# Optimization experiments

Hardware: AMD Instinct MI355X
Metric: run time of the kernel (lower is better)

The kernel has to match this reference:

```python
import jax, jax.numpy as jnp
import numpy as np

N, E, CIN, CHID, DIM, KS = 6000, 192000, 32, 64, 3, 5
K = KS ** DIM          # 125 total spline kernel weights
S = 2 ** DIM           # 8 nonzero linear B-spline basis products per edge


def spline_conv(x, edge_index, pseudo, W, root, bias):
    """SplineConv, degree-1 open B-spline, mean aggregation, root weight + bias.
    x: [N, Cin], edge_index: [2, E], pseudo: [E, DIM] in [0,1],
    W: [K, Cin, Cout], root: [Cin, Cout], bias: [Cout].
    """
    src, dst = edge_index[0], edge_index[1]
    cin = x.shape[1]
    # open spline: KS-1 intervals over [0,1]
    u = pseudo * (KS - 1)                               # [E, DIM]
    i0 = jnp.clip(jnp.floor(u), 0, KS - 2).astype(jnp.int32)
    frac = u - i0                                       # [E, DIM]
    bits = (jnp.arange(S)[:, None] >> jnp.arange(DIM)[None, :]) & 1   # [S, DIM]
    strides = KS ** jnp.arange(DIM - 1, -1, -1)         # row-major flattening
    idx = jnp.sum((i0[:, None, :] + bits[None, :, :]) * strides, axis=-1)  # [E, S]
    basis = jnp.prod(jnp.where(bits[None, :, :] == 1,
                               frac[:, None, :], 1.0 - frac[:, None, :]), axis=-1)  # [E, S]
    x_j = x[src]                                        # gather: [E, Cin]
    vals = (basis[..., None] * x_j[:, None, :]).reshape(E * S, cin)
    keys = (dst[:, None] * K + idx).reshape(E * S)
    # bucket basis-weighted source features per (dst node, kernel index)
    T = jax.ops.segment_sum(vals, keys, num_segments=N * K).reshape(N, K, cin)
    out = jnp.einsum('nki,kio->no', T, W)               # [N, Cout]
    deg = jax.ops.segment_sum(jnp.ones((E,), jnp.float32), dst, num_segments=N)
    out = out / jnp.maximum(deg, 1.0)[:, None]          # mean aggregation
    return out + x @ root + bias


def _conv_params(key, cin):
    k1, k2 = jax.random.split(key)
    w_scale = 1.0 / np.sqrt(cin * S)
    W = jax.random.normal(k1, (K, cin, CHID), jnp.float32) * w_scale
    root = jax.random.normal(k2, (cin, CHID), jnp.float32) * (1.0 / np.sqrt(cin))
    b = jnp.zeros((CHID,), jnp.float32)
    return W, root, b


def setup_inputs() -> dict:
    key = jax.random.key(0)
    ks = jax.random.split(key, 10)
    inp = {
        'x': jax.random.normal(ks[0], (N, CIN), jnp.float32),
        'hidden': jax.random.normal(ks[1], (N, CHID), jnp.float32),
        'edge_index': jax.random.randint(ks[2], (2, E), 0, N, dtype=jnp.int32),
        'edge_attr': jax.random.uniform(ks[3], (E, DIM), jnp.float32),
    }
    for i, (name, cin) in enumerate([('xr', CIN), ('hr', CHID), ('xz', CIN),
                                     ('hz', CHID), ('xn', CIN), ('hn', CHID)]):
        W, root, b = _conv_params(ks[4 + i], cin)
        inp[f'W_{name}'] = W
        inp[f'root_{name}'] = root
        inp[f'b_{name}'] = b
    return inp


def reference(x, hidden, edge_index, edge_attr,
              W_xr, root_xr, b_xr, W_hr, root_hr, b_hr,
              W_xz, root_xz, b_xz, W_hz, root_hz, b_hz,
              W_xn, root_xn, b_xn, W_hn, root_hn, b_hn):
    hr_out = spline_conv(hidden, edge_index, edge_attr, W_hr, root_hr, b_hr)
    r = jax.nn.sigmoid(spline_conv(x, edge_index, edge_attr, W_xr, root_xr, b_xr) + hr_out)
    z = jax.nn.sigmoid(spline_conv(x, edge_index, edge_attr, W_xz, root_xz, b_xz)
                       + spline_conv(hidden, edge_index, edge_attr, W_hz, root_hz, b_hz))
    # NOTE: the original torch forward reuses self.hr (not self.hn) here; replicated faithfully.
    n = jnp.tanh(spline_conv(x, edge_index, edge_attr, W_xn, root_xn, b_xn) + r * hr_out)
    h_new = (1.0 - z) * n + z * hidden
    return h_new
```

## Files before the change

kernel.cpp:

```cpp
#include <hip/hip_runtime.h>
#include <math.h>

#define NN_   6000
#define EE_   192000
#define CIN_  32
#define CHID_ 64
#define KK_   125
#define EB_   32
#define CH1_  4
#define CH2_  8
#define CPB_  16
#define MTILE_ 192

static __device__ __forceinline__ unsigned short f2bf(float f) {
    unsigned int u = __builtin_bit_cast(unsigned int, f);
    u += 0x7fff + ((u >> 16) & 1);
    return (unsigned short)(u >> 16);
}
static __device__ __forceinline__ float bf2f(unsigned short h) {
    unsigned int u = ((unsigned int)h) << 16;
    return __builtin_bit_cast(float, u);
}

template<int N> static __device__ __forceinline__ void vwait() {
    asm volatile("s_waitcnt vmcnt(%0)" :: "n"(N) : "memory");
    __builtin_amdgcn_sched_barrier(0);
}

#define PK1_ (192 * KK_ * CIN_)
#define PK2_ (128 * KK_ * CHID_)
#define CB_  ((EE_ + 255) / 256)
__global__ __launch_bounds__(256) void count_pack_kernel(
    const int* __restrict__ ei, int* __restrict__ deg,
    const float* __restrict__ W_xr, const float* __restrict__ W_xz,
    const float* __restrict__ W_xn, const float* __restrict__ W_hr,
    const float* __restrict__ W_hz,
    unsigned short* __restrict__ B1t, unsigned short* __restrict__ B2t)
{
    const int b = blockIdx.x;
    if (b < CB_) {
        int e = b * 256 + threadIdx.x;
        if (e < EE_) atomicAdd(&deg[ei[EE_ + e]], 1);
        return;
    }
    int gid = (b - CB_) * 256 + threadIdx.x;
    if (gid < PK1_) {
        int n  = gid / (KK_ * CIN_);
        int kk = gid % (KK_ * CIN_);
        int conv = n >> 6, o = n & 63;
        const float* W = (conv == 0) ? W_xr : ((conv == 1) ? W_xz : W_xn);
        B1t[gid] = f2bf(W[(size_t)kk * 64 + o]);
    } else if (gid < PK1_ + PK2_) {
        int g2 = gid - PK1_;
        int n  = g2 / (KK_ * CHID_);
        int kk = g2 % (KK_ * CHID_);
        int conv = n >> 6, o = n & 63;
        const float* W = (conv == 0) ? W_hr : W_hz;
        B2t[g2] = f2bf(W[(size_t)kk * 64 + o]);
    }
}

__global__ __launch_bounds__(1024) void scan_kernel(
    const int* __restrict__ deg, int* __restrict__ offs, int* __restrict__ cursor)
{
    __shared__ int part[1024];
    const int tid = threadIdx.x;
    const int CH = (NN_ + 1023) / 1024;
    const int base = tid * CH;
    int loc[CH];
    int s = 0;
#pragma unroll
    for (int i = 0; i < CH; ++i) {
        int v = (base + i < NN_) ? deg[base + i] : 0;
        loc[i] = s; s += v;
    }
    part[tid] = s;
    __syncthreads();
    for (int off = 1; off < 1024; off <<= 1) {
        int v = (tid >= off) ? part[tid - off] : 0;
        __syncthreads();
        part[tid] += v;
        __syncthreads();
    }
    const int pre = (tid > 0) ? part[tid - 1] : 0;
#pragma unroll
    for (int i = 0; i < CH; ++i) {
        if (base + i < NN_) {
            offs[base + i]   = pre + loc[i];
            cursor[base + i] = pre + loc[i];
        }
    }
    if (tid == 1023) offs[NN_] = part[1023];
}

__global__ __launch_bounds__(256) void prep_kernel(
    const int* __restrict__ ei, const float* __restrict__ attr,
    int* __restrict__ cursor, float4* __restrict__ meta_s, int* __restrict__ src_s)
{
    int e = blockIdx.x * 256 + threadIdx.x;
    if (e >= EE_) return;
    const int dst = ei[EE_ + e];
    const int p   = atomicAdd(&cursor[dst], 1);
    float f[3]; int i0[3];
#pragma unroll
    for (int d = 0; d < 3; ++d) {
        float u  = attr[e * 3 + d] * 4.0f;
        float fl = floorf(u);
        fl = fminf(fmaxf(fl, 0.0f), 3.0f);
        i0[d] = (int)fl;
        f[d]  = u - fl;
    }
    meta_s[p] = make_float4(f[0], f[1], f[2],
        __int_as_float(i0[0] * 25 + i0[1] * 5 + i0[2]));
    src_s[p] = ei[e];
}

template<int C>
__global__ __launch_bounds__(256) void build_T_kernel(
    const float4* __restrict__ meta_s, const int* __restrict__ src_s,
    const float* __restrict__ feat, const int* __restrict__ offs,
    unsigned short* __restrict__ Tb)
{
    constexpr int MP  = 40;
    constexpr int CT  = C / 16;
    constexpr int CPT = C / 8;
    using bf16x8 = __attribute__((ext_vector_type(8))) short;
    using f32x4  = __attribute__((ext_vector_type(4))) float;

    __shared__ __align__(16) unsigned short Mt [128 * MP];
    __shared__ __align__(16) unsigned short fbT[C   * MP];
    __shared__ int s_src[EB_];

    const int tid  = threadIdx.x;
    const int wave = tid >> 6;
    const int lane = tid & 63;
    const int quad = lane >> 4;
    const int l16  = lane & 15;
    const int node = blockIdx.x;

    for (int i = tid; i < C * MP / 8; i += 256)
        ((uint4*)fbT)[i] = make_uint4(0u, 0u, 0u, 0u);

    const int j0 = offs[node], j1 = offs[node + 1];

    f32x4 acc[2][CT];
#pragma unroll
    for (int t = 0; t < 2; ++t)
#pragma unroll
        for (int ct = 0; ct < CT; ++ct) acc[t][ct] = (f32x4){0.f, 0.f, 0.f, 0.f};

    for (int jb = j0; jb < j1; jb += EB_) {
        const int m = min(EB_, j1 - jb);

        __syncthreads();
        for (int i = tid; i < 128 * MP / 8; i += 256)
            ((uint4*)Mt)[i] = make_uint4(0u, 0u, 0u, 0u);
        if (tid < m) s_src[tid] = src_s[jb + tid];
        __syncthreads();

        if (tid < m) {
            const float4 mt = meta_s[jb + tid];
            const int base = __float_as_int(mt.w);
            const float f0 = mt.x, f1 = mt.y, f2 = mt.z;
            const float g0 = 1.f - f0, g1 = 1.f - f1, g2 = 1.f - f2;
            const float bb[8] = {g0*g1*g2, f0*g1*g2, g0*f1*g2, f0*f1*g2,
                                 g0*g1*f2, f0*g1*f2, g0*f1*f2, f0*f1*f2};
            const int oc[8] = {0, 25, 5, 30, 1, 26, 6, 31};
#pragma unroll
            for (int s = 0; s < 8; ++s)
                Mt[(base + oc[s]) * MP + tid] = f2bf(bb[s]);
        }
        {
            const int e = tid >> 3, cg = (tid & 7) * CPT;
            if (e < m) {
                const float* fr = &feat[(size_t)s_src[e] * C + cg];
#pragma unroll
                for (int c4 = 0; c4 < CPT; c4 += 4) {
                    float4 v = *(const float4*)(fr + c4);
                    fbT[(cg + c4 + 0) * MP + e] = f2bf(v.x);
                    fbT[(cg + c4 + 1) * MP + e] = f2bf(v.y);
                    fbT[(cg + c4 + 2) * MP + e] = f2bf(v.z);
                    fbT[(cg + c4 + 3) * MP + e] = f2bf(v.w);
                }
            }
        }
        __syncthreads();

        bf16x8 a0 = *(const bf16x8*)&Mt[((wave * 2 + 0) * 16 + l16) * MP + quad * 8];
        bf16x8 a1 = *(const bf16x8*)&Mt[((wave * 2 + 1) * 16 + l16) * MP + quad * 8];
#pragma unroll
        for (int ct = 0; ct < CT; ++ct) {
            bf16x8 b = *(const bf16x8*)&fbT[(ct * 16 + l16) * MP + quad * 8];
            acc[0][ct] = __builtin_amdgcn_mfma_f32_16x16x32_bf16(a0, b, acc[0][ct], 0, 0, 0);
            acc[1][ct] = __builtin_amdgcn_mfma_f32_16x16x32_bf16(a1, b, acc[1][ct], 0, 0, 0);
        }
    }

    unsigned short* To = Tb + (size_t)node * (KK_ * C);
#pragma unroll
    for (int t = 0; t < 2; ++t) {
        const int rbase = (wave * 2 + t) * 16 + quad * 4;
#pragma unroll
        for (int ct = 0; ct < CT; ++ct) {
#pragma unroll
            for (int r = 0; r < 4; ++r) {
                const int R = rbase + r;
                if (R < KK_) To[R * C + ct * 16 + l16] = f2bf(acc[t][ct][r]);
            }
        }
    }
}

template<int NT, int NTF, int CPB, int LW>
static __device__ __forceinline__ void gemm_body(
    unsigned short* arena,
    const unsigned short* __restrict__ A, const unsigned short* __restrict__ Bt,
    const unsigned short* __restrict__ zp,
    unsigned short* __restrict__ P, int M, int Kd, int chunk, int zhalf)
{
    constexpr int COLS   = 64;
    constexpr int RF     = 3;
    constexpr int NFRAG  = NT / 16;
    constexpr int CSP    = NT + 8;
    constexpr int ASH    = MTILE_ * COLS;
    constexpr int SLOT   = ASH + 128 * COLS;
    constexpr int AUNITS = MTILE_ * COLS / 8;
    constexpr int BUNITS = NT * COLS / 8;

    using bf16x8 = __attribute__((ext_vector_type(8))) short;
    using f32x4  = __attribute__((ext_vector_type(4))) float;

    const int tid  = threadIdx.x;
    const int wave = tid >> 6;
    const int lane = tid & 63;
    const int quad = lane >> 4;
    const int l16  = lane & 15;
    const int m0   = blockIdx.x * MTILE_;
    const unsigned short* Bp = Bt + (size_t)zhalf * NT * Kd;
    const int kbase = chunk * CPB * COLS;
    const int ccmax = min(CPB, (Kd - kbase + COLS - 1) / COLS);

    f32x4 acc[RF][NFRAG];
#pragma unroll
    for (int t = 0; t < RF; ++t)
#pragma unroll
        for (int f = 0; f < NFRAG; ++f) acc[t][f] = (f32x4){0.f, 0.f, 0.f, 0.f};

    auto STAGE = [&](int cc, int slot) {
        unsigned short* Abuf = arena + slot * SLOT;
        unsigned short* Bbuf = Abuf + ASH;
        const int k0 = kbase + cc * COLS;
#pragma unroll
        for (int i = 0; i < AUNITS / 256; ++i) {
            const int u    = tid + i * 256;
            const int row  = u >> 3;
            const int gblk = (u & 7) ^ (row & 7);
            const int k    = k0 + gblk * 8;
            const unsigned short* g = (k + 8 <= Kd)
                ? A + (size_t)(m0 + row) * Kd + k
                : zp + (u & 3) * 8;
            __builtin_amdgcn_global_load_lds(
                (const __attribute__((address_space(1))) void*)g,
                (__attribute__((address_space(3))) void*)(Abuf + u * 8),
                16, 0, 0);
        }
#pragma unroll
        for (int i = 0; i < BUNITS / 256; ++i) {
            const int u    = tid + i * 256;
            const int row  = u >> 3;
            const int gblk = (u & 7) ^ (row & 7);
            const unsigned short* g = Bp + (size_t)row * Kd + k0 + gblk * 8;
            __builtin_amdgcn_global_load_lds(
                (const __attribute__((address_space(1))) void*)g,
                (__attribute__((address_space(3))) void*)(Bbuf + u * 8),
                16, 0, 0);
        }
    };

    STAGE(0, 0);
    STAGE(1, 1);

    for (int cc = 0; cc < ccmax; ++cc) {
        asm volatile("" ::: "memory");
        __builtin_amdgcn_s_barrier();
        if (cc + 2 < ccmax) STAGE(cc + 2, (cc + 2) % 3);
        const int ahead = min(2, ccmax - 1 - cc);
        if      (ahead == 2) vwait<2 * LW>();
        else if (ahead == 1) vwait<LW>();
        else                 vwait<0>();
        __builtin_amdgcn_s_barrier();
        asm volatile("" ::: "memory");

        const unsigned short* Ac = arena + (cc % 3) * SLOT;
        const unsigned short* Bc = Ac + ASH;
#pragma unroll
        for (int s = 0; s < 2; ++s) {
            bf16x8 av[RF];
#pragma unroll
            for (int t = 0; t < RF; ++t) {
                const int row = (wave * RF + t) * 16 + l16;
                av[t] = *(const bf16x8*)
                    &Ac[row * COLS + (((s * 4 + quad) ^ (l16 & 7)) * 8)];
            }
#pragma unroll
            for (int f = 0; f < NFRAG; ++f) {
                bf16x8 bv = *(const bf16x8*)
                    &Bc[(f * 16 + l16) * COLS + (((s * 4 + quad) ^ (l16 & 7)) * 8)];
#pragma unroll
                for (int t = 0; t < RF; ++t)
                    acc[t][f] = __builtin_amdgcn_mfma_f32_16x16x32_bf16(
                        av[t], bv, acc[t][f], 0, 0, 0);
            }
        }
    }

    unsigned short* Cs = arena;
    unsigned short* Pc = P + ((size_t)chunk * M + m0) * NTF + zhalf * NT;
#pragma unroll
    for (int p = 0; p < 3; ++p) {
        __syncthreads();
#pragma unroll
        for (int t = 0; t < RF; ++t) {
            const int fr = wave * RF + t;
            if ((fr >> 2) == p) {
                const int rb = (fr & 3) * 16 + quad * 4;
#pragma unroll
                for (int f = 0; f < NFRAG; ++f) {
                    const int col = f * 16 + l16;
#pragma unroll
                    for (int r = 0; r < 4; ++r)
                        Cs[(rb + r) * CSP + col] = f2bf(acc[t][f][r]);
                }
            }
        }
        __syncthreads();
        constexpr int UNITS = 64 * NT / 8;
        for (int u = tid; u < UNITS; u += 256) {
            const int row = (u * 8) / NT, col = (u * 8) % NT;
            if (m0 + p * 64 + row < M)
                *(uint4*)&Pc[(size_t)(p * 64 + row) * NTF + col] =
                    *(const uint4*)&Cs[row * CSP + col];
        }
    }
}

__global__ __launch_bounds__(256) void gemm_all_kernel(
    const unsigned short* __restrict__ Tx, const unsigned short* __restrict__ B1t,
    unsigned short* __restrict__ P1,
    const unsigned short* __restrict__ Th, const unsigned short* __restrict__ B2t,
    unsigned short* __restrict__ P2, const unsigned short* __restrict__ zp)
{
    __shared__ __align__(16) unsigned short arena[3 * 20480];
    const int y = blockIdx.y;
    if (y < CH2_) {
        gemm_body<128, 128, CPB_, 10>(arena, Th, B2t, zp, P2, NN_, KK_ * CHID_, y, 0);
    } else {
        const int g = y - CH2_;
        gemm_body<96, 192, CPB_, 9>(arena, Tx, B1t, zp, P1, NN_, KK_ * CIN_, g >> 1, g & 1);
    }
}

__global__ __launch_bounds__(256) void epilogue_kernel(
    const unsigned short* __restrict__ P1, const unsigned short* __restrict__ P2,
    const int* __restrict__ offs,
    const float* __restrict__ x, const float* __restrict__ hidden,
    const float* __restrict__ root_xr, const float* __restrict__ root_hr,
    const float* __restrict__ root_xz, const float* __restrict__ root_hz,
    const float* __restrict__ root_xn,
    const float* __restrict__ b_xr, const float* __restrict__ b_hr,
    const float* __restrict__ b_xz, const float* __restrict__ b_hz,
    const float* __restrict__ b_xn,
    float* __restrict__ out)
{
    __shared__ float xsh[4][32];
    __shared__ float hsh[4][64];
    const int w = threadIdx.x >> 6;
    const int o = threadIdx.x & 63;
    const int m = blockIdx.x * 4 + w;
    if (m >= NN_) return;

    if (o < 32) xsh[w][o] = x[(size_t)m * 32 + o];
    const float hval = hidden[(size_t)m * 64 + o];
    hsh[w][o] = hval;

    float axr = 0.f, axz = 0.f, axn = 0.f;
#pragma unroll
    for (int c = 0; c < CH1_; ++c) {
        const unsigned short* p = P1 + ((size_t)c * NN_ + m) * 192;
        axr += bf2f(p[o]); axz += bf2f(p[64 + o]); axn += bf2f(p[128 + o]);
    }
    float ahr = 0.f, ahz = 0.f;
#pragma unroll
    for (int c = 0; c < CH2_; ++c) {
        const unsigned short* p = P2 + ((size_t)c * NN_ + m) * 128;
        ahr += bf2f(p[o]); ahz += bf2f(p[64 + o]);
    }

    const int   dg   = offs[m + 1] - offs[m];
    const float dinv = 1.0f / fmaxf((float)dg, 1.0f);
    axr *= dinv; axz *= dinv; axn *= dinv; ahr *= dinv; ahz *= dinv;

    float sxr = 0.f, sxz = 0.f, sxn = 0.f;
#pragma unroll
    for (int c = 0; c < CIN_; ++c) {
        float xv = xsh[w][c];
        sxr += xv * root_xr[c * 64 + o];
        sxz += xv * root_xz[c * 64 + o];
        sxn += xv * root_xn[c * 64 + o];
    }
    float shr = 0.f, shz = 0.f;
#pragma unroll
    for (int c = 0; c < CHID_; ++c) {
        float hv = hsh[w][c];
        shr += hv * root_hr[c * 64 + o];
        shz += hv * root_hz[c * 64 + o];
    }

    const float conv_xr = axr + sxr + b_xr[o];
    const float conv_xz = axz + sxz + b_xz[o];
    const float conv_xn = axn + sxn + b_xn[o];
    const float hr_out  = ahr + shr + b_hr[o];
    const float conv_hz = ahz + shz + b_hz[o];

    const float rg = 1.0f / (1.0f + expf(-(conv_xr + hr_out)));
    const float zg = 1.0f / (1.0f + expf(-(conv_xz + conv_hz)));
    const float ng = tanhf(conv_xn + rg * hr_out);
    out[(size_t)m * 64 + o] = (1.0f - zg) * ng + zg * hval;
}

extern "C" void kernel_launch(void* const* d_in, const int* in_sizes, int n_in,
                              void* d_out, int out_size, void* d_ws, size_t ws_size,
                              hipStream_t stream)
{
    const float* x       = (const float*)d_in[0];
    const float* hidden  = (const float*)d_in[1];
    const int*   ei      = (const int*)  d_in[2];
    const float* attr    = (const float*)d_in[3];
    const float* W_xr    = (const float*)d_in[4];
    const float* root_xr = (const float*)d_in[5];
    const float* b_xr    = (const float*)d_in[6];
    const float* W_hr    = (const float*)d_in[7];
    const float* root_hr = (const float*)d_in[8];
    const float* b_hr    = (const float*)d_in[9];
    const float* W_xz    = (const float*)d_in[10];
    const float* root_xz = (const float*)d_in[11];
    const float* b_xz    = (const float*)d_in[12];
    const float* W_hz    = (const float*)d_in[13];
    const float* root_hz = (const float*)d_in[14];
    const float* b_hz    = (const float*)d_in[15];
    const float* W_xn    = (const float*)d_in[16];
    const float* root_xn = (const float*)d_in[17];
    const float* b_xn    = (const float*)d_in[18];
    float* out = (float*)d_out;

    char* w = (char*)d_ws;
    unsigned short* Tx  = (unsigned short*)w; w += (size_t)NN_ * KK_ * CIN_  * 2;
    unsigned short* Th  = (unsigned short*)w; w += (size_t)NN_ * KK_ * CHID_ * 2;
    unsigned short* B1t = (unsigned short*)w; w += (size_t)192 * KK_ * CIN_  * 2;
    unsigned short* B2t = (unsigned short*)w; w += (size_t)128 * KK_ * CHID_ * 2;
    unsigned short* P1  = (unsigned short*)w; w += (size_t)CH1_ * NN_ * 192 * 2;
    unsigned short* P2  = (unsigned short*)w; w += (size_t)CH2_ * NN_ * 128 * 2;
    float4* meta_s = (float4*)w; w += (size_t)EE_ * 16;
    int* src_s  = (int*)w;   w += (size_t)EE_ * 4;
    int* deg    = (int*)w;   w += (size_t)NN_ * 4;
    int* offs   = (int*)w;   w += (size_t)(NN_ + 4) * 4;
    int* cursor = (int*)w;   w += (size_t)NN_ * 4;
    unsigned short* zpad = (unsigned short*)w; w += 256;

    const int MT = (NN_ + MTILE_ - 1) / MTILE_;

    hipMemsetAsync(deg, 0, (size_t)NN_ * 4, stream);
    hipMemsetAsync(zpad, 0, 256, stream);

    const int PACKB = (PK1_ + PK2_ + 255) / 256;
    count_pack_kernel<<<CB_ + PACKB, 256, 0, stream>>>(
        ei, deg, W_xr, W_xz, W_xn, W_hr, W_hz, B1t, B2t);

    scan_kernel<<<1, 1024, 0, stream>>>(deg, offs, cursor);
    prep_kernel<<<(EE_ + 255) / 256, 256, 0, stream>>>(ei, attr, cursor, meta_s, src_s);

    build_T_kernel<CHID_><<<NN_, 256, 0, stream>>>(meta_s, src_s, hidden, offs, Th);
    build_T_kernel<CIN_><<<NN_, 256, 0, stream>>>(meta_s, src_s, x, offs, Tx);

    gemm_all_kernel<<<dim3(MT, CH2_ + 2 * CH1_), 256, 0, stream>>>(
        Tx, B1t, P1, Th, B2t, P2, zpad);

    epilogue_kernel<<<(NN_ + 3) / 4, 256, 0, stream>>>(
        P1, P2, offs, x, hidden,
        root_xr, root_hr, root_xz, root_hz, root_xn,
        b_xr, b_hr, b_xz, b_hz, b_xn, out);
}
```

Baseline: 245.2 us.

## Pad atomic counters, parallelize basis scatter, switch GEMM to double-buffered pipeline

Degree and cursor counters are spaced 16 ints apart so the atomics for neighbouring nodes stop contending on the same cache line. In build_T, basis weights are first staged in shared memory, and the 8 scatter writes per edge are spread over 8 threads instead of one loop per thread; one barrier is merged away. The GEMM moves from a 3-slot to a 2-slot LDS pipeline with one stage of prefetch, adds s_setprio around the MFMA section, and adds a trailing barrier. This cuts LDS use (possibly raising occupancy) but shortens the prefetch distance, and the padding adds a larger memset.

```diff
diff --git a/kernel.cpp b/kernel.cpp
--- a/kernel.cpp
+++ b/kernel.cpp
@@ -11,6 +11,7 @@
 #define CH2_  8
 #define CPB_  16
 #define MTILE_ 192
+#define DSTR_ 16
 
 static __device__ __forceinline__ unsigned short f2bf(float f) {
     unsigned int u = __builtin_bit_cast(unsigned int, f);
@@ -40,7 +41,7 @@
     const int b = blockIdx.x;
     if (b < CB_) {
         int e = b * 256 + threadIdx.x;
-        if (e < EE_) atomicAdd(&deg[ei[EE_ + e]], 1);
+        if (e < EE_) atomicAdd(&deg[ei[EE_ + e] * DSTR_], 1);
         return;
     }
     int gid = (b - CB_) * 256 + threadIdx.x;
@@ -71,7 +72,7 @@
     int s = 0;
 #pragma unroll
     for (int i = 0; i < CH; ++i) {
-        int v = (base + i < NN_) ? deg[base + i] : 0;
+        int v = (base + i < NN_) ? deg[(base + i) * DSTR_] : 0;
         loc[i] = s; s += v;
     }
     part[tid] = s;
@@ -86,8 +87,8 @@
 #pragma unroll
     for (int i = 0; i < CH; ++i) {
         if (base + i < NN_) {
-            offs[base + i]   = pre + loc[i];
-            cursor[base + i] = pre + loc[i];
+            offs[base + i]            = pre + loc[i];
+            cursor[(base + i) * DSTR_] = pre + loc[i];
         }
     }
     if (tid == 1023) offs[NN_] = part[1023];
@@ -100,7 +101,7 @@
     int e = blockIdx.x * 256 + threadIdx.x;
     if (e >= EE_) return;
     const int dst = ei[EE_ + e];
-    const int p   = atomicAdd(&cursor[dst], 1);
+    const int p   = atomicAdd(&cursor[dst * DSTR_], 1);
     float f[3]; int i0[3];
 #pragma unroll
     for (int d = 0; d < 3; ++d) {
@@ -129,7 +130,9 @@
 
     __shared__ __align__(16) unsigned short Mt [128 * MP];
     __shared__ __align__(16) unsigned short fbT[C   * MP];
-    __shared__ int s_src[EB_];
+    __shared__ int   s_src[EB_];
+    __shared__ int   s_cell[EB_];
+    __shared__ float s_basis[EB_ * 8];
 
     const int tid  = threadIdx.x;
     const int wave = tid >> 6;
@@ -155,20 +158,26 @@
         __syncthreads();
         for (int i = tid; i < 128 * MP / 8; i += 256)
             ((uint4*)Mt)[i] = make_uint4(0u, 0u, 0u, 0u);
-        if (tid < m) s_src[tid] = src_s[jb + tid];
-        __syncthreads();
-
         if (tid < m) {
             const float4 mt = meta_s[jb + tid];
-            const int base = __float_as_int(mt.w);
+            s_src[tid]  = src_s[jb + tid];
+            s_cell[tid] = __float_as_int(mt.w);
             const float f0 = mt.x, f1 = mt.y, f2 = mt.z;
             const float g0 = 1.f - f0, g1 = 1.f - f1, g2 = 1.f - f2;
-            const float bb[8] = {g0*g1*g2, f0*g1*g2, g0*f1*g2, f0*f1*g2,
-                                 g0*g1*f2, f0*g1*f2, g0*f1*f2, f0*f1*f2};
-            const int oc[8] = {0, 25, 5, 30, 1, 26, 6, 31};
-#pragma unroll
-            for (int s = 0; s < 8; ++s)
-                Mt[(base + oc[s]) * MP + tid] = f2bf(bb[s]);
+            float4 blo = make_float4(g0*g1*g2, f0*g1*g2, g0*f1*g2, f0*f1*g2);
+            float4 bhi = make_float4(g0*g1*f2, f0*g1*f2, g0*f1*f2, f0*f1*f2);
+            *(float4*)&s_basis[tid * 8]     = blo;
+            *(float4*)&s_basis[tid * 8 + 4] = bhi;
+        }
+        __syncthreads();
+
+        {
+            const int e = tid >> 3, s = tid & 7;
+            if (e < m) {
+                const int cell = s_cell[e] + 25 * (s & 1)
+                               + 5 * ((s >> 1) & 1) + ((s >> 2) & 1);
+                Mt[cell * MP + e] = f2bf(s_basis[e * 8 + s]);
+            }
         }
         {
             const int e = tid >> 3, cg = (tid & 7) * CPT;
@@ -278,21 +287,16 @@
     };
 
     STAGE(0, 0);
-    STAGE(1, 1);
 
     for (int cc = 0; cc < ccmax; ++cc) {
-        asm volatile("" ::: "memory");
-        __builtin_amdgcn_s_barrier();
-        if (cc + 2 < ccmax) STAGE(cc + 2, (cc + 2) % 3);
-        const int ahead = min(2, ccmax - 1 - cc);
-        if      (ahead == 2) vwait<2 * LW>();
-        else if (ahead == 1) vwait<LW>();
-        else                 vwait<0>();
+        if (cc + 1 < ccmax) { STAGE(cc + 1, (cc + 1) & 1); vwait<LW>(); }
+        else                { vwait<0>(); }
         __builtin_amdgcn_s_barrier();
         asm volatile("" ::: "memory");
 
-        const unsigned short* Ac = arena + (cc % 3) * SLOT;
+        const unsigned short* Ac = arena + (cc & 1) * SLOT;
         const unsigned short* Bc = Ac + ASH;
+        __builtin_amdgcn_s_setprio(1);
 #pragma unroll
         for (int s = 0; s < 2; ++s) {
             bf16x8 av[RF];
@@ -312,6 +316,10 @@
                         av[t], bv, acc[t][f], 0, 0, 0);
             }
         }
+        __builtin_amdgcn_s_setprio(0);
+        asm volatile("" ::: "memory");
+        __builtin_amdgcn_s_barrier();
+        asm volatile("" ::: "memory");
     }
 
     unsigned short* Cs = arena;
@@ -350,7 +358,7 @@
     const unsigned short* __restrict__ Th, const unsigned short* __restrict__ B2t,
     unsigned short* __restrict__ P2, const unsigned short* __restrict__ zp)
 {
-    __shared__ __align__(16) unsigned short arena[3 * 20480];
+    __shared__ __align__(16) unsigned short arena[2 * 20480];
     const int y = blockIdx.y;
     if (y < CH2_) {
         gemm_body<128, 128, CPB_, 10>(arena, Th, B2t, zp, P2, NN_, KK_ * CHID_, y, 0);
@@ -462,14 +470,14 @@
     unsigned short* P2  = (unsigned short*)w; w += (size_t)CH2_ * NN_ * 128 * 2;
     float4* meta_s = (float4*)w; w += (size_t)EE_ * 16;
     int* src_s  = (int*)w;   w += (size_t)EE_ * 4;
-    int* deg    = (int*)w;   w += (size_t)NN_ * 4;
+    int* deg    = (int*)w;   w += (size_t)NN_ * DSTR_ * 4;
     int* offs   = (int*)w;   w += (size_t)(NN_ + 4) * 4;
-    int* cursor = (int*)w;   w += (size_t)NN_ * 4;
+    int* cursor = (int*)w;   w += (size_t)NN_ * DSTR_ * 4;
     unsigned short* zpad = (unsigned short*)w; w += 256;
 
     const int MT = (NN_ + MTILE_ - 1) / MTILE_;
 
-    hipMemsetAsync(deg, 0, (size_t)NN_ * 4, stream);
+    hipMemsetAsync(deg, 0, (size_t)NN_ * DSTR_ * 4, stream);
     hipMemsetAsync(zpad, 0, 256, stream);
 
     const int PACKB = (PK1_ + PK2_ + 255) / 256;
```

Result: no change. 250.1 us (+2.0%).

## Shrink GEMM M-tile to 128 with double buffering and tile-transpose weight packing

Applied to the files above, without the earlier changes.

The GEMM M-tile drops from 192 to 128 rows (RF 3 to 2) and the LDS pipeline goes from three stages to two, so the arena shrinks and occupancy or block count can rise. MFMA sections are wrapped in s_setprio, and an extra barrier now ends each k-iteration. Separately, weight packing now transposes 64-row tiles through shared memory with coalesced float4 reads and uint4 writes, replacing the strided per-element gather. The trade-off is less prefetch depth and more barriers in exchange for more parallel blocks.

```diff
diff --git a/kernel.cpp b/kernel.cpp
--- a/kernel.cpp
+++ b/kernel.cpp
@@ -10,7 +10,7 @@
 #define CH1_  4
 #define CH2_  8
 #define CPB_  16
-#define MTILE_ 192
+#define MTILE_ 128
 
 static __device__ __forceinline__ unsigned short f2bf(float f) {
     unsigned int u = __builtin_bit_cast(unsigned int, f);
@@ -27,8 +27,11 @@
     __builtin_amdgcn_sched_barrier(0);
 }
 
-#define PK1_ (192 * KK_ * CIN_)
-#define PK2_ (128 * KK_ * CHID_)
+#define RX_  (KK_ * CIN_)
+#define RH_  (KK_ * CHID_)
+#define NB1_ ((RX_ + 63) / 64)
+#define NB2_ (RH_ / 64)
+#define PACKB_ (3 * NB1_ + 2 * NB2_)
 #define CB_  ((EE_ + 255) / 256)
 __global__ __launch_bounds__(256) void count_pack_kernel(
     const int* __restrict__ ei, int* __restrict__ deg,
@@ -37,26 +40,49 @@
     const float* __restrict__ W_hz,
     unsigned short* __restrict__ B1t, unsigned short* __restrict__ B2t)
 {
+    __shared__ float ts[64][65];
     const int b = blockIdx.x;
+    const int tid = threadIdx.x;
     if (b < CB_) {
-        int e = b * 256 + threadIdx.x;
+        int e = b * 256 + tid;
         if (e < EE_) atomicAdd(&deg[ei[EE_ + e]], 1);
         return;
     }
-    int gid = (b - CB_) * 256 + threadIdx.x;
-    if (gid < PK1_) {
-        int n  = gid / (KK_ * CIN_);
-        int kk = gid % (KK_ * CIN_);
-        int conv = n >> 6, o = n & 63;
-        const float* W = (conv == 0) ? W_xr : ((conv == 1) ? W_xz : W_xn);
-        B1t[gid] = f2bf(W[(size_t)kk * 64 + o]);
-    } else if (gid < PK1_ + PK2_) {
-        int g2 = gid - PK1_;
-        int n  = g2 / (KK_ * CHID_);
-        int kk = g2 % (KK_ * CHID_);
-        int conv = n >> 6, o = n & 63;
-        const float* W = (conv == 0) ? W_hr : W_hz;
-        B2t[g2] = f2bf(W[(size_t)kk * 64 + o]);
+    const int pid = b - CB_;
+    const float* W;
+    unsigned short* Bo;
+    int r0, Rv, RL;
+    if (pid < 3 * NB1_) {
+        const int conv = pid / NB1_, rb = pid % NB1_;
+        W  = (conv == 0) ? W_xr : ((conv == 1) ? W_xz : W_xn);
+        Bo = B1t + (size_t)(conv * 64) * RX_;
+        r0 = rb * 64; Rv = min(64, RX_ - r0); RL = RX_;
+    } else {
+        const int p2 = pid - 3 * NB1_;
+        const int conv = p2 / NB2_, rb = p2 % NB2_;
+        W  = (conv == 0) ? W_hr : W_hz;
+        Bo = B2t + (size_t)(conv * 64) * RH_;
+        r0 = rb * 64; Rv = 64; RL = RH_;
+    }
+    for (int u = tid; u < Rv * 16; u += 256) {
+        const int row = u >> 4, c4 = u & 15;
+        float4 v = ((const float4*)(W + (size_t)(r0 + row) * 64))[c4];
+        ts[row][c4 * 4 + 0] = v.x; ts[row][c4 * 4 + 1] = v.y;
+        ts[row][c4 * 4 + 2] = v.z; ts[row][c4 * 4 + 3] = v.w;
+    }
+    __syncthreads();
+    const int G = Rv >> 3;
+    for (int u = tid; u < 64 * G; u += 256) {
+        const int o = u / G, g = u % G;
+        unsigned int w4[4];
+#pragma unroll
+        for (int j = 0; j < 4; ++j) {
+            unsigned int lo = f2bf(ts[g * 8 + 2 * j][o]);
+            unsigned int hi = f2bf(ts[g * 8 + 2 * j + 1][o]);
+            w4[j] = lo | (hi << 16);
+        }
+        *(uint4*)&Bo[(size_t)o * RL + r0 + g * 8] =
+            make_uint4(w4[0], w4[1], w4[2], w4[3]);
     }
 }
 
@@ -219,13 +245,14 @@
     unsigned short* __restrict__ P, int M, int Kd, int chunk, int zhalf)
 {
     constexpr int COLS   = 64;
-    constexpr int RF     = 3;
+    constexpr int RF     = 2;
     constexpr int NFRAG  = NT / 16;
     constexpr int CSP    = NT + 8;
     constexpr int ASH    = MTILE_ * COLS;
     constexpr int SLOT   = ASH + 128 * COLS;
     constexpr int AUNITS = MTILE_ * COLS / 8;
     constexpr int BUNITS = NT * COLS / 8;
+    constexpr int NPASS  = MTILE_ / 64;
 
     using bf16x8 = __attribute__((ext_vector_type(8))) short;
     using f32x4  = __attribute__((ext_vector_type(4))) float;
@@ -278,21 +305,16 @@
     };
 
     STAGE(0, 0);
-    STAGE(1, 1);
 
     for (int cc = 0; cc < ccmax; ++cc) {
-        asm volatile("" ::: "memory");
-        __builtin_amdgcn_s_barrier();
-        if (cc + 2 < ccmax) STAGE(cc + 2, (cc + 2) % 3);
-        const int ahead = min(2, ccmax - 1 - cc);
-        if      (ahead == 2) vwait<2 * LW>();
-        else if (ahead == 1) vwait<LW>();
-        else                 vwait<0>();
+        if (cc + 1 < ccmax) { STAGE(cc + 1, (cc + 1) & 1); vwait<LW>(); }
+        else                { vwait<0>(); }
         __builtin_amdgcn_s_barrier();
         asm volatile("" ::: "memory");
 
-        const unsigned short* Ac = arena + (cc % 3) * SLOT;
+        const unsigned short* Ac = arena + (cc & 1) * SLOT;
         const unsigned short* Bc = Ac + ASH;
+        __builtin_amdgcn_s_setprio(1);
 #pragma unroll
         for (int s = 0; s < 2; ++s) {
             bf16x8 av[RF];
@@ -312,12 +334,16 @@
                         av[t], bv, acc[t][f], 0, 0, 0);
             }
         }
+        __builtin_amdgcn_s_setprio(0);
+        asm volatile("" ::: "memory");
+        __builtin_amdgcn_s_barrier();
+        asm volatile("" ::: "memory");
     }
 
     unsigned short* Cs = arena;
     unsigned short* Pc = P + ((size_t)chunk * M + m0) * NTF + zhalf * NT;
 #pragma unroll
-    for (int p = 0; p < 3; ++p) {
+    for (int p = 0; p < NPASS; ++p) {
         __syncthreads();
 #pragma unroll
         for (int t = 0; t < RF; ++t) {
@@ -350,13 +376,13 @@
     const unsigned short* __restrict__ Th, const unsigned short* __restrict__ B2t,
     unsigned short* __restrict__ P2, const unsigned short* __restrict__ zp)
 {
-    __shared__ __align__(16) unsigned short arena[3 * 20480];
+    __shared__ __align__(16) unsigned short arena[2 * 16384];
     const int y = blockIdx.y;
     if (y < CH2_) {
-        gemm_body<128, 128, CPB_, 10>(arena, Th, B2t, zp, P2, NN_, KK_ * CHID_, y, 0);
+        gemm_body<128, 128, CPB_, 8>(arena, Th, B2t, zp, P2, NN_, KK_ * CHID_, y, 0);
     } else {
         const int g = y - CH2_;
-        gemm_body<96, 192, CPB_, 9>(arena, Tx, B1t, zp, P1, NN_, KK_ * CIN_, g >> 1, g & 1);
+        gemm_body<96, 192, CPB_, 7>(arena, Tx, B1t, zp, P1, NN_, KK_ * CIN_, g >> 1, g & 1);
     }
 }
 
@@ -472,8 +498,7 @@
     hipMemsetAsync(deg, 0, (size_t)NN_ * 4, stream);
     hipMemsetAsync(zpad, 0, 256, stream);
 
-    const int PACKB = (PK1_ + PK2_ + 255) / 256;
-    count_pack_kernel<<<CB_ + PACKB, 256, 0, stream>>>(
+    count_pack_kernel<<<CB_ + PACKB_, 256, 0, stream>>>(
         ei, deg, W_xr, W_xz, W_xn, W_hr, W_hz, B1t, B2t);
 
     scan_kernel<<<1, 1024, 0, stream>>>(deg, offs, cursor);
```

Result: no change. 242.6 us, median of 2 (-1.1%).
